# Kernel tuning notes

Hardware: AMD Instinct MI355X
Metric: run time of the kernel (lower is better)

The kernel has to match this reference:

```python
import jax, jax.numpy as jnp
import numpy as np

# ---- sign binarization with straight-through estimator (standard BNN) ----
@jax.custom_vjp
def binarize(x):
    return jnp.where(x >= 0, 1.0, -1.0).astype(x.dtype)

def _bin_fwd(x):
    return binarize(x), x

def _bin_bwd(x, g):
    return (g * (jnp.abs(x) <= 1.0).astype(g.dtype),)

binarize.defvjp(_bin_fwd, _bin_bwd)

def conv2d(x, w):
    # x: [N,C,H,W], w: [O,I,kh,kw], stride 1, VALID padding (padding=0)
    return jax.lax.conv_general_dilated(
        x, w, window_strides=(1, 1), padding='VALID',
        dimension_numbers=('NCHW', 'OIHW', 'NCHW'))

def maxpool2(x):
    return jax.lax.reduce_window(x, -jnp.inf, jax.lax.max,
                                 (1, 1, 2, 2), (1, 1, 2, 2), 'VALID')

def hardtanh(x):
    return jnp.clip(x, -1.0, 1.0)

def setup_inputs() -> dict:
    key = jax.random.key(0)
    ks = jax.random.split(key, 11)
    B = 8192
    s = 0.1
    return {
        'x':   jax.random.normal(ks[0], (B, 3, 32, 32), jnp.float32),
        'w1':  jax.random.normal(ks[1], (6, 3, 5, 5), jnp.float32) * s,
        'b1':  jax.random.normal(ks[2], (6,), jnp.float32) * s,
        'w2':  jax.random.normal(ks[3], (16, 6, 5, 5), jnp.float32) * s,
        'b2':  jax.random.normal(ks[4], (16,), jnp.float32) * s,
        'wf1': jax.random.normal(ks[5], (120, 400), jnp.float32) * s,
        'bf1': jax.random.normal(ks[6], (120,), jnp.float32) * s,
        'wf2': jax.random.normal(ks[7], (84, 120), jnp.float32) * s,
        'bf2': jax.random.normal(ks[8], (84,), jnp.float32) * s,
        'wf3': jax.random.normal(ks[9], (10, 84), jnp.float32) * s,
        'bf3': jax.random.normal(ks[10], (10,), jnp.float32) * s,
    }

def reference(x, w1, b1, w2, b2, wf1, bf1, wf2, bf2, wf3, bf3):
    # conv1: first layer -> real-valued input, binarized weights
    out = conv2d(x, binarize(w1)) + b1[None, :, None, None]   # [B,6,28,28]
    out = maxpool2(hardtanh(out))                              # [B,6,14,14]
    # conv2: binarized input and weights
    out = conv2d(binarize(out), binarize(w2)) + b2[None, :, None, None]  # [B,16,10,10]
    out = maxpool2(hardtanh(out))                              # [B,16,5,5]
    out = out.reshape(out.shape[0], -1)                        # [B,400]
    out = hardtanh(binarize(out) @ binarize(wf1).T + bf1)      # [B,120]
    out = hardtanh(binarize(out) @ binarize(wf2).T + bf2)      # [B,84]
    out = binarize(out) @ binarize(wf3).T + bf3                # [B,10]
    return out
```

## Files before the change

kernel.cpp:

```cpp
#include <hip/hip_runtime.h>
#include <stdint.h>

#define TPB 256
#define RCAP 128
#define BAND 0.05f

#define WS_BFR   0
#define WS_W1B   1024
#define WS_W2PK  1042
#define WS_WF1P  1122
#define WS_WF2PK 4122
#define WS_WF3PK 4458

typedef _Float16 half8 __attribute__((ext_vector_type(8)));
typedef float f32x4 __attribute__((ext_vector_type(4)));
typedef unsigned int u32x4 __attribute__((ext_vector_type(4)));

__device__ __forceinline__ uint32_t pkf16(float a, float b) {
  uint32_t lo = (uint32_t)__builtin_bit_cast(uint16_t, (_Float16)a);
  uint32_t hi = (uint32_t)__builtin_bit_cast(uint16_t, (_Float16)b);
  return lo | (hi << 16);
}

__device__ __forceinline__ double win_sum(const float* __restrict__ xb,
                                          uint32_t b0, uint32_t b1, uint32_t b2) {
  double s = 0.0;
#pragma unroll
  for (int ic = 0; ic < 3; ++ic)
#pragma unroll
    for (int rr = 0; rr < 5; ++rr) {
      const float* rp = xb + ic * 1024 + rr * 32;
#pragma unroll
      for (int kc = 0; kc < 5; ++kc) {
        const int idx = ic * 25 + rr * 5 + kc;
        const uint32_t bw = (idx < 32) ? b0 : ((idx < 64) ? b1 : b2);
        double xv = (double)rp[kc];
        s += ((bw >> (idx & 31)) & 1u) ? xv : -xv;
      }
    }
  return s;
}

__global__ __launch_bounds__(TPB) void prep_kernel(
    const float* __restrict__ w1, const float* __restrict__ w2,
    const float* __restrict__ wf1, const float* __restrict__ wf2,
    const float* __restrict__ wf3, uint32_t* __restrict__ wsu)
{
  int id = blockIdx.x * TPB + threadIdx.x;
  if (id < 1024) {
    int s = id >> 8, r = id & 255, ln = r >> 2, dw = r & 3;
    int g4 = ln >> 4, n = ln & 15;
    int o = 4*s + g4, kr = o / 3, kcp = o % 3;
    uint32_t w = 0;
    for (int h = 0; h < 2; ++h) {
      int j = dw*2 + h;
      int kcin = j >> 2, ic = j & 3, kc = kcp*2 + kcin;
      uint32_t f = 0;
      if (o < 15 && n < 6 && ic < 3 && kc < 5)
        f = (w1[(n*3 + ic)*25 + kr*5 + kc] >= 0.f) ? 0x3C00u : 0xBC00u;
      w |= f << (16*h);
    }
    wsu[WS_BFR + id] = w;
  } else if (id < 1042) {
    int i = id - 1024, c = i / 3, q = i % 3;
    uint32_t w = 0;
    for (int b = 0; b < 32; ++b) {
      int k = q * 32 + b;
      if (k < 75) w |= (uint32_t)(w1[c*75 + k] >= 0.f) << b;
    }
    wsu[WS_W1B + i] = w;
  } else if (id < 1122) {
    int r = id - 1042, oc = r / 5, kr = r % 5;
    uint32_t w = 0;
    for (int c = 0; c < 6; ++c)
      for (int k = 0; k < 5; ++k)
        w |= (uint32_t)(w2[((oc*6 + c)*5 + kr)*5 + k] >= 0.f) << (5*c + k);
    wsu[WS_W2PK + r] = w;
  } else if (id < 4122) {
    int r = id - 1122, o = r / 25, p = r % 25;
    uint32_t w = 0;
    for (int oc = 0; oc < 16; ++oc)
      w |= (uint32_t)(wf1[o*400 + oc*25 + p] >= 0.f) << oc;
    wsu[WS_WF1P + r] = w;
  } else if (id < 4458) {
    int r = id - 4122, o = r / 4, q = r % 4;
    uint32_t w = 0;
    for (int b = 0; b < 32; ++b) {
      int n = q*32 + b;
      if (n < 120) w |= (uint32_t)(wf2[o*120 + n] >= 0.f) << b;
    }
    wsu[WS_WF2PK + r] = w;
  } else if (id < 4488) {
    int r = id - 4458, o = r / 3, q = r % 3;
    uint32_t w = 0;
    for (int b = 0; b < 32; ++b) {
      int n = q*32 + b;
      if (n < 84) w |= (uint32_t)(wf3[o*84 + n] >= 0.f) << b;
    }
    wsu[WS_WF3PK + r] = w;
  }
}

__global__ void __launch_bounds__(TPB, 4) lenet_kernel(
    const float* __restrict__ x,
    const float* __restrict__ b1, const float* __restrict__ b2,
    const float* __restrict__ bf1, const float* __restrict__ bf2,
    const float* __restrict__ bf3,
    const uint32_t* __restrict__ wsu,
    float* __restrict__ out, int imgs_total)
{
  __shared__ __align__(16) union Ovl {
    uint32_t imgh[8712];
    uint32_t ppatch[4][10][10][5];
  } ovl;
  __shared__ uint32_t w1bs[18];
  __shared__ float sb1[6];
  __shared__ float sb2[16];
  __shared__ uint32_t bits1[4][6][14];
  __shared__ uint32_t border_[4][6][14];
  __shared__ uint32_t w2pks[16][5];
  __shared__ uint32_t bits2[4][25];
  __shared__ uint32_t wf2pks[84][4];
  __shared__ uint32_t wf3pks[10][3];
  __shared__ uint32_t bitsf1[4][4];
  __shared__ uint32_t bitsf2[4][3];
  __shared__ uint32_t rlist[RCAP];
  __shared__ int rcnt;

  const int t = threadIdx.x;
  const int lane = t & 63;
  const int wv = t >> 6;
  const int m16 = lane & 15;
  const int g4 = lane >> 4;
  const long long img0 = (long long)blockIdx.x * 4;
  const int nimg = (img0 + 4 <= imgs_total) ? 4 : (int)(imgs_total - img0);

  {
    const int im = t >> 6, y = (t >> 1) & 31, xh = t & 1;
    if (im < nimg) {
      const float* rp = x + (img0 + im) * 3072 + y * 32 + xh * 16;
      const int pixbase = (im * 33 + y) * 33 + xh * 16;
#pragma unroll
      for (int q = 0; q < 4; ++q) {
        float4 f0 = *(const float4*)(rp +    0 + 4 * q);
        float4 f1 = *(const float4*)(rp + 1024 + 4 * q);
        float4 f2 = *(const float4*)(rp + 2048 + 4 * q);
        uint32_t* d = &ovl.imgh[2 * (pixbase + 4 * q)];
        *(uint2*)(d + 0) = make_uint2(pkf16(f0.x, f1.x), pkf16(f2.x, 0.f));
        *(uint2*)(d + 2) = make_uint2(pkf16(f0.y, f1.y), pkf16(f2.y, 0.f));
        *(uint2*)(d + 4) = make_uint2(pkf16(f0.z, f1.z), pkf16(f2.z, 0.f));
        *(uint2*)(d + 6) = make_uint2(pkf16(f0.w, f1.w), pkf16(f2.w, 0.f));
      }
    }
    for (int id = t; id < 260; id += TPB) {
      int pix;
      if (id < 132) { int i2 = id / 33, k = id % 33; pix = (i2 * 33 + 32) * 33 + k; }
      else { int r = id - 132; int i2 = r >> 5, yy = r & 31; pix = (i2 * 33 + yy) * 33 + 32; }
      *(uint2*)&ovl.imgh[2 * pix] = make_uint2(0u, 0u);
    }
    if (t < 18) w1bs[t] = wsu[WS_W1B + t];
    if (t < 6)  sb1[t] = b1[t];
    if (t >= 8 && t < 24) sb2[t - 8] = b2[t - 8];
    if (t < 80) w2pks[t / 5][t % 5] = wsu[WS_W2PK + t];
    if (t < 168) {
      ((uint32_t*)wf2pks)[t]       = wsu[WS_WF2PK + t];
      ((uint32_t*)wf2pks)[t + 168] = wsu[WS_WF2PK + t + 168];
    }
    if (t < 30) ((uint32_t*)wf3pks)[t] = wsu[WS_WF3PK + t];
    for (int id = t; id < 336; id += TPB) {
      ((uint32_t*)bits1)[id] = 0; ((uint32_t*)border_)[id] = 0;
    }
    if (t < 100) ((uint32_t*)bits2)[t] = 0;
    if (t < 16) ((uint32_t*)bitsf1)[t] = 0;
    if (t < 12) ((uint32_t*)bitsf2)[t] = 0;
    if (t == 0) rcnt = 0;
  }
  __syncthreads();

  if (wv < nimg) {
    u32x4 bf[4];
#pragma unroll
    for (int s = 0; s < 4; ++s)
      bf[s] = *(const u32x4*)&wsu[WS_BFR + (s << 8) + (lane << 2)];
    const float bcr = sb1[(m16 < 6) ? m16 : 0];
    int koffs[4];
#pragma unroll
    for (int s = 0; s < 4; ++s) {
      const int o = 4 * s + g4;
      koffs[s] = (o / 3) * 33 + (o % 3) * 2;
    }
    const int imbase = wv * 33 * 33;
    for (int pyi = 0; pyi < 14; ++pyi) {
#pragma unroll
      for (int xg = 0; xg < 2; ++xg) {
        const int pb = imbase + (2 * pyi) * 33 + xg * 12 + m16;
        f32x4 a0 = {0.f, 0.f, 0.f, 0.f}, a1 = {0.f, 0.f, 0.f, 0.f};
#pragma unroll
        for (int s = 0; s < 4; ++s) {
          const uint2* p = (const uint2*)&ovl.imgh[2 * (pb + koffs[s])];
          uint2 r0 = p[0], r1 = p[1];
          uint2 r2 = p[33], r3 = p[34];
          u32x4 wa = {r0.x, r0.y, r1.x, r1.y};
          u32x4 wb = {r2.x, r2.y, r3.x, r3.y};
          a0 = __builtin_amdgcn_mfma_f32_16x16x32_f16(
                 __builtin_bit_cast(half8, wa), __builtin_bit_cast(half8, bf[s]), a0, 0, 0, 0);
          a1 = __builtin_amdgcn_mfma_f32_16x16x32_f16(
                 __builtin_bit_cast(half8, wb), __builtin_bit_cast(half8, bf[s]), a1, 0, 0, 0);
        }
        if (m16 < 6) {
          float v0 = fmaxf(fmaxf(a0[0], a0[1]), fmaxf(a1[0], a1[1])) + bcr;
          float v1 = fmaxf(fmaxf(a0[2], a0[3]), fmaxf(a1[2], a1[3])) + bcr;
          const int px = xg * 6 + g4 * 2;
          uint32_t nib = 0, nb = 0;
          if (fabsf(v0) < BAND) nb |= 1u << px; else if (v0 >= 0.f) nib |= 1u << px;
          if (fabsf(v1) < BAND) nb |= 1u << (px + 1); else if (v1 >= 0.f) nib |= 1u << (px + 1);
          if (nib) atomicOr(&bits1[wv][m16][pyi], nib);
          if (nb)  atomicOr(&border_[wv][m16][pyi], nb);
        }
      }
    }
  }
  __syncthreads();

  for (int id = t; id < 336; id += TPB) {
    uint32_t bw = ((uint32_t*)border_)[id];
    while (bw) {
      int pj = __ffs(bw) - 1;
      bw &= bw - 1;
      int slot = atomicAdd(&rcnt, 1);
      if (slot < RCAP) rlist[slot] = (uint32_t)(id * 16 + pj);
    }
  }
  __syncthreads();

  {
    const int cnt = min(rcnt, RCAP);
    for (int k = t; k < cnt * 4; k += TPB) {
      const int e = k >> 2, win = k & 3;
      const uint32_t ent = rlist[e];
      const int pj = ent & 15, w = ent >> 4;
      const int pi = w % 14, c = (w / 14) % 6, im = w / 84;
      const int dr = win >> 1, dc = win & 1;
      const float* xb = x + (img0 + im) * 3072 + (2*pi + dr) * 32 + (2*pj + dc);
      double s = win_sum(xb, w1bs[c*3], w1bs[c*3+1], w1bs[c*3+2]);
      double s1 = fmax(s, __shfl_xor(s, 1));
      double sm = fmax(s1, __shfl_xor(s1, 2));
      if (win == 0) {
        if (sm + (double)sb1[c] >= 0.0)
          atomicOr(&((uint32_t*)bits1)[w], 1u << pj);
      }
    }
    if (rcnt > RCAP) {
      for (int id = t; id < 4704; id += TPB) {
        const int w = id / 14, pj = id % 14;
        if ((((uint32_t*)border_)[w] >> pj) & 1u) {
          const int pi = w % 14, c = (w / 14) % 6, im = w / 84;
          double best = -1e300;
          for (int dr = 0; dr < 2; ++dr)
            for (int dc = 0; dc < 2; ++dc) {
              const float* xb = x + (img0 + im) * 3072 + (2*pi + dr) * 32 + (2*pj + dc);
              double s = win_sum(xb, w1bs[c*3], w1bs[c*3+1], w1bs[c*3+2]);
              best = best > s ? best : s;
            }
          if (best + (double)sb1[c] >= 0.0)
            atomicOr(&((uint32_t*)bits1)[w], 1u << pj);
        }
      }
    }
  }
  __syncthreads();

  for (int id = t; id < 2000; id += TPB) {
    const int im  = id / 500;
    const int rem = id % 500;
    const int kr = rem % 5;
    const int ij = rem / 5;
    const int i = ij / 10, j = ij % 10;
    uint32_t w = 0;
#pragma unroll
    for (int c = 0; c < 6; ++c)
      w |= ((bits1[im][c][i + kr] >> j) & 31u) << (5*c);
    ovl.ppatch[im][i][j][kr] = w;
  }
  __syncthreads();

  for (int id = t; id < 1600; id += TPB) {
    const int im  = id / 400;
    const int rem = id % 400;
    const int oc  = rem / 25;
    const int pos = rem % 25;
    const int pi = pos / 5, pj = pos % 5;
    int dmin = 1000;
#pragma unroll
    for (int dy = 0; dy < 2; ++dy)
#pragma unroll
      for (int dx = 0; dx < 2; ++dx) {
        const uint32_t* pp = ovl.ppatch[im][2*pi + dy][2*pj + dx];
        int d = 0;
#pragma unroll
        for (int kr = 0; kr < 5; ++kr) d += __popc(pp[kr] ^ w2pks[oc][kr]);
        dmin = min(dmin, d);
      }
    float v = (float)(150 - 2*dmin) + sb2[oc];
    if (v >= 0.f) atomicOr(&bits2[im][pos], 1u << oc);
  }
  __syncthreads();

  for (int id = t; id < 480; id += TPB) {
    const int im = id / 120;
    const int o = id % 120;
    const uint32_t* wrow = wsu + WS_WF1P + o*25;
    int d = 0;
#pragma unroll
    for (int p = 0; p < 25; ++p) d += __popc(bits2[im][p] ^ wrow[p]);
    float v = (float)(400 - 2*d) + bf1[o];
    if (v >= 0.f) atomicOr(&bitsf1[im][o >> 5], 1u << (o & 31));
  }
  __syncthreads();

  for (int id = t; id < 336; id += TPB) {
    const int im = id / 84;
    const int o = id % 84;
    int d = 0;
#pragma unroll
    for (int q = 0; q < 4; ++q) d += __popc(bitsf1[im][q] ^ wf2pks[o][q]);
    float v = (float)(120 - 2*d) + bf2[o];
    if (v >= 0.f) atomicOr(&bitsf2[im][o >> 5], 1u << (o & 31));
  }
  __syncthreads();

  for (int id = t; id < 40; id += TPB) {
    const int im = id / 10;
    const int o = id % 10;
    if (im < nimg) {
      int d = 0;
#pragma unroll
      for (int q = 0; q < 3; ++q) d += __popc(bitsf2[im][q] ^ wf3pks[q == 0 ? o : o][q]);
      out[(img0 + im)*10 + o] = (float)(84 - 2*d) + bf3[o];
    }
  }
}

extern "C" void kernel_launch(void* const* d_in, const int* in_sizes, int n_in,
                              void* d_out, int out_size, void* d_ws, size_t ws_size,
                              hipStream_t stream)
{
  const float* x   = (const float*)d_in[0];
  const float* w1  = (const float*)d_in[1];
  const float* b1  = (const float*)d_in[2];
  const float* w2  = (const float*)d_in[3];
  const float* b2  = (const float*)d_in[4];
  const float* wf1 = (const float*)d_in[5];
  const float* bf1 = (const float*)d_in[6];
  const float* wf2 = (const float*)d_in[7];
  const float* bf2 = (const float*)d_in[8];
  const float* wf3 = (const float*)d_in[9];
  const float* bf3 = (const float*)d_in[10];
  uint32_t* wsu = (uint32_t*)d_ws;

  const int imgs = in_sizes[0] / 3072;
  hipLaunchKernelGGL(prep_kernel, dim3(18), dim3(TPB), 0, stream,
                     w1, w2, wf1, wf2, wf3, wsu);
  const int nblk = (imgs + 3) / 4;
  hipLaunchKernelGGL(lenet_kernel, dim3(nblk), dim3(TPB), 0, stream,
                     x, b1, b2, bf1, bf2, bf3, wsu, (float*)d_out, imgs);
}
```

Measured before the change: 73.88 us.

## Remap conv1 MFMA to cover both pool rows, shrink image LDS padding

Conv1's MFMA B-matrix is reorganised so that each of the 16 columns covers a channel and a vertical pool offset (12 used). Every MFMA K-step now spans 6 kernel rows, giving 5 steps per row pair instead of 4 with two row shifts, and one pass per pooled row instead of two x-groups. Horizontal pooling and bit assembly use wave shuffles, and the shared-memory atomicOr calls become plain stores from one lane per channel. The image buffer drops its padding row, which reduces LDS use. In exchange, MFMA column utilisation falls slightly (12 of 16) and shuffle work is added.

Measured after the change: 69.91 us. -5.4%, faster.

```diff
diff --git a/kernel.cpp b/kernel.cpp
--- a/kernel.cpp
+++ b/kernel.cpp
@@ -6,11 +6,11 @@
 #define BAND 0.05f
 
 #define WS_BFR   0
-#define WS_W1B   1024
-#define WS_W2PK  1042
-#define WS_WF1P  1122
-#define WS_WF2PK 4122
-#define WS_WF3PK 4458
+#define WS_W1B   1280
+#define WS_W2PK  1298
+#define WS_WF1P  1378
+#define WS_WF2PK 4378
+#define WS_WF3PK 4714
 
 typedef _Float16 half8 __attribute__((ext_vector_type(8)));
 typedef float f32x4 __attribute__((ext_vector_type(4)));
@@ -47,51 +47,52 @@
     const float* __restrict__ wf3, uint32_t* __restrict__ wsu)
 {
   int id = blockIdx.x * TPB + threadIdx.x;
-  if (id < 1024) {
+  if (id < 1280) {
     int s = id >> 8, r = id & 255, ln = r >> 2, dw = r & 3;
     int g4 = ln >> 4, n = ln & 15;
-    int o = 4*s + g4, kr = o / 3, kcp = o % 3;
+    int o = 4 * s + g4, r6 = o / 3, cp = o % 3;
+    int c = n >> 1, dy = n & 1;
     uint32_t w = 0;
     for (int h = 0; h < 2; ++h) {
-      int j = dw*2 + h;
-      int kcin = j >> 2, ic = j & 3, kc = kcp*2 + kcin;
+      int j2 = dw * 2 + h;
+      int ic = j2 & 3, pix = j2 >> 2, kc = cp * 2 + pix, kr = r6 - dy;
       uint32_t f = 0;
-      if (o < 15 && n < 6 && ic < 3 && kc < 5)
-        f = (w1[(n*3 + ic)*25 + kr*5 + kc] >= 0.f) ? 0x3C00u : 0xBC00u;
-      w |= f << (16*h);
+      if (n < 12 && o < 18 && ic < 3 && kc < 5 && kr >= 0 && kr <= 4)
+        f = (w1[(c * 3 + ic) * 25 + kr * 5 + kc] >= 0.f) ? 0x3C00u : 0xBC00u;
+      w |= f << (16 * h);
     }
     wsu[WS_BFR + id] = w;
-  } else if (id < 1042) {
-    int i = id - 1024, c = i / 3, q = i % 3;
+  } else if (id < 1298) {
+    int i = id - 1280, c = i / 3, q = i % 3;
     uint32_t w = 0;
     for (int b = 0; b < 32; ++b) {
       int k = q * 32 + b;
       if (k < 75) w |= (uint32_t)(w1[c*75 + k] >= 0.f) << b;
     }
     wsu[WS_W1B + i] = w;
-  } else if (id < 1122) {
-    int r = id - 1042, oc = r / 5, kr = r % 5;
+  } else if (id < 1378) {
+    int r = id - 1298, oc = r / 5, kr = r % 5;
     uint32_t w = 0;
     for (int c = 0; c < 6; ++c)
       for (int k = 0; k < 5; ++k)
         w |= (uint32_t)(w2[((oc*6 + c)*5 + kr)*5 + k] >= 0.f) << (5*c + k);
     wsu[WS_W2PK + r] = w;
-  } else if (id < 4122) {
-    int r = id - 1122, o = r / 25, p = r % 25;
+  } else if (id < 4378) {
+    int r = id - 1378, o = r / 25, p = r % 25;
     uint32_t w = 0;
     for (int oc = 0; oc < 16; ++oc)
       w |= (uint32_t)(wf1[o*400 + oc*25 + p] >= 0.f) << oc;
     wsu[WS_WF1P + r] = w;
-  } else if (id < 4458) {
-    int r = id - 4122, o = r / 4, q = r % 4;
+  } else if (id < 4714) {
+    int r = id - 4378, o = r / 4, q = r % 4;
     uint32_t w = 0;
     for (int b = 0; b < 32; ++b) {
       int n = q*32 + b;
       if (n < 120) w |= (uint32_t)(wf2[o*120 + n] >= 0.f) << b;
     }
     wsu[WS_WF2PK + r] = w;
-  } else if (id < 4488) {
-    int r = id - 4458, o = r / 3, q = r % 3;
+  } else if (id < 4744) {
+    int r = id - 4714, o = r / 3, q = r % 3;
     uint32_t w = 0;
     for (int b = 0; b < 32; ++b) {
       int n = q*32 + b;
@@ -110,7 +111,7 @@
     float* __restrict__ out, int imgs_total)
 {
   __shared__ __align__(16) union Ovl {
-    uint32_t imgh[8712];
+    uint32_t imgh[8448];
     uint32_t ppatch[4][10][10][5];
   } ovl;
   __shared__ uint32_t w1bs[18];
@@ -139,7 +140,7 @@
     const int im = t >> 6, y = (t >> 1) & 31, xh = t & 1;
     if (im < nimg) {
       const float* rp = x + (img0 + im) * 3072 + y * 32 + xh * 16;
-      const int pixbase = (im * 33 + y) * 33 + xh * 16;
+      const int pixbase = (im * 32 + y) * 33 + xh * 16;
 #pragma unroll
       for (int q = 0; q < 4; ++q) {
         float4 f0 = *(const float4*)(rp +    0 + 4 * q);
@@ -152,11 +153,9 @@
         *(uint2*)(d + 6) = make_uint2(pkf16(f0.w, f1.w), pkf16(f2.w, 0.f));
       }
     }
-    for (int id = t; id < 260; id += TPB) {
-      int pix;
-      if (id < 132) { int i2 = id / 33, k = id % 33; pix = (i2 * 33 + 32) * 33 + k; }
-      else { int r = id - 132; int i2 = r >> 5, yy = r & 31; pix = (i2 * 33 + yy) * 33 + 32; }
-      *(uint2*)&ovl.imgh[2 * pix] = make_uint2(0u, 0u);
+    for (int id = t; id < 128; id += TPB) {
+      int i2 = id >> 5, yy = id & 31;
+      *(uint2*)&ovl.imgh[2 * ((i2 * 32 + yy) * 33 + 32)] = make_uint2(0u, 0u);
     }
     if (t < 18) w1bs[t] = wsu[WS_W1B + t];
     if (t < 6)  sb1[t] = b1[t];
@@ -178,45 +177,55 @@
   __syncthreads();
 
   if (wv < nimg) {
-    u32x4 bf[4];
-#pragma unroll
-    for (int s = 0; s < 4; ++s)
+    u32x4 bf[5];
+#pragma unroll
+    for (int s = 0; s < 5; ++s)
       bf[s] = *(const u32x4*)&wsu[WS_BFR + (s << 8) + (lane << 2)];
-    const float bcr = sb1[(m16 < 6) ? m16 : 0];
-    int koffs[4];
-#pragma unroll
-    for (int s = 0; s < 4; ++s) {
+    int koffs[5];
+#pragma unroll
+    for (int s = 0; s < 5; ++s) {
       const int o = 4 * s + g4;
-      koffs[s] = (o / 3) * 33 + (o % 3) * 2;
-    }
-    const int imbase = wv * 33 * 33;
+      koffs[s] = (o < 18) ? (o / 3) * 33 + (o % 3) * 2 : 0;
+    }
+    const int n = m16;
+    const int c = n >> 1;
+    const float bcr = sb1[(n < 12) ? c : 0];
     for (int pyi = 0; pyi < 14; ++pyi) {
-#pragma unroll
-      for (int xg = 0; xg < 2; ++xg) {
-        const int pb = imbase + (2 * pyi) * 33 + xg * 12 + m16;
-        f32x4 a0 = {0.f, 0.f, 0.f, 0.f}, a1 = {0.f, 0.f, 0.f, 0.f};
-#pragma unroll
-        for (int s = 0; s < 4; ++s) {
-          const uint2* p = (const uint2*)&ovl.imgh[2 * (pb + koffs[s])];
-          uint2 r0 = p[0], r1 = p[1];
-          uint2 r2 = p[33], r3 = p[34];
-          u32x4 wa = {r0.x, r0.y, r1.x, r1.y};
-          u32x4 wb = {r2.x, r2.y, r3.x, r3.y};
-          a0 = __builtin_amdgcn_mfma_f32_16x16x32_f16(
-                 __builtin_bit_cast(half8, wa), __builtin_bit_cast(half8, bf[s]), a0, 0, 0, 0);
-          a1 = __builtin_amdgcn_mfma_f32_16x16x32_f16(
-                 __builtin_bit_cast(half8, wb), __builtin_bit_cast(half8, bf[s]), a1, 0, 0, 0);
-        }
-        if (m16 < 6) {
-          float v0 = fmaxf(fmaxf(a0[0], a0[1]), fmaxf(a1[0], a1[1])) + bcr;
-          float v1 = fmaxf(fmaxf(a0[2], a0[3]), fmaxf(a1[2], a1[3])) + bcr;
-          const int px = xg * 6 + g4 * 2;
-          uint32_t nib = 0, nb = 0;
-          if (fabsf(v0) < BAND) nb |= 1u << px; else if (v0 >= 0.f) nib |= 1u << px;
-          if (fabsf(v1) < BAND) nb |= 1u << (px + 1); else if (v1 >= 0.f) nib |= 1u << (px + 1);
-          if (nib) atomicOr(&bits1[wv][m16][pyi], nib);
-          if (nb)  atomicOr(&border_[wv][m16][pyi], nb);
-        }
+      const int rowpix = (wv * 32 + 2 * pyi) * 33 + m16;
+      f32x4 aX = {0.f, 0.f, 0.f, 0.f}, aY = {0.f, 0.f, 0.f, 0.f};
+#pragma unroll
+      for (int s = 0; s < 5; ++s) {
+        const uint2* pX = (const uint2*)&ovl.imgh[2 * (rowpix + koffs[s])];
+        const uint2* pY = (const uint2*)&ovl.imgh[2 * (rowpix + 12 + koffs[s])];
+        uint2 x0 = pX[0], x1 = pX[1];
+        uint2 y0 = pY[0], y1 = pY[1];
+        u32x4 wa = {x0.x, x0.y, x1.x, x1.y};
+        u32x4 wb = {y0.x, y0.y, y1.x, y1.y};
+        aX = __builtin_amdgcn_mfma_f32_16x16x32_f16(
+               __builtin_bit_cast(half8, wa), __builtin_bit_cast(half8, bf[s]), aX, 0, 0, 0);
+        aY = __builtin_amdgcn_mfma_f32_16x16x32_f16(
+               __builtin_bit_cast(half8, wb), __builtin_bit_cast(half8, bf[s]), aY, 0, 0, 0);
+      }
+      float pX0 = fmaxf(aX[0], aX[1]), pX1 = fmaxf(aX[2], aX[3]);
+      float pY0 = fmaxf(aY[0], aY[1]), pY1 = fmaxf(aY[2], aY[3]);
+      float qX0 = fmaxf(pX0, __shfl_xor(pX0, 1));
+      float qX1 = fmaxf(pX1, __shfl_xor(pX1, 1));
+      float qY0 = fmaxf(pY0, __shfl_xor(pY0, 1));
+      float qY1 = fmaxf(pY1, __shfl_xor(pY1, 1));
+      uint32_t comb = 0;
+      {
+        float v0 = qX0 + bcr, v1 = qX1 + bcr, v2 = qY0 + bcr, v3 = qY1 + bcr;
+        const int p0 = g4 * 2, p1 = g4 * 2 + 1, p2 = 6 + g4 * 2, p3 = 7 + g4 * 2;
+        if (fabsf(v0) < BAND) comb |= 1u << (16 + p0); else if (v0 >= 0.f) comb |= 1u << p0;
+        if (fabsf(v1) < BAND) comb |= 1u << (16 + p1); else if (v1 >= 0.f) comb |= 1u << p1;
+        if (fabsf(v2) < BAND) comb |= 1u << (16 + p2); else if (v2 >= 0.f) comb |= 1u << p2;
+        if (fabsf(v3) < BAND) comb |= 1u << (16 + p3); else if (v3 >= 0.f) comb |= 1u << p3;
+      }
+      comb |= __shfl_xor(comb, 16);
+      comb |= __shfl_xor(comb, 32);
+      if (g4 == 0 && n < 12 && (n & 1) == 0) {
+        bits1[wv][c][pyi]   = comb & 0x3FFFu;
+        border_[wv][c][pyi] = comb >> 16;
       }
     }
   }
@@ -335,7 +344,7 @@
     if (im < nimg) {
       int d = 0;
 #pragma unroll
-      for (int q = 0; q < 3; ++q) d += __popc(bitsf2[im][q] ^ wf3pks[q == 0 ? o : o][q]);
+      for (int q = 0; q < 3; ++q) d += __popc(bitsf2[im][q] ^ wf3pks[o][q]);
       out[(img0 + im)*10 + o] = (float)(84 - 2*d) + bf3[o];
     }
   }
@@ -359,7 +368,7 @@
   uint32_t* wsu = (uint32_t*)d_ws;
 
   const int imgs = in_sizes[0] / 3072;
-  hipLaunchKernelGGL(prep_kernel, dim3(18), dim3(TPB), 0, stream,
+  hipLaunchKernelGGL(prep_kernel, dim3(19), dim3(TPB), 0, stream,
                      w1, w2, wf1, wf2, wf3, wsu);
   const int nblk = (imgs + 3) / 4;
   hipLaunchKernelGGL(lenet_kernel, dim3(nblk), dim3(TPB), 0, stream,
```
